# Optimization experiments

Measured on AMD Instinct MI355X. Metric: run time of the kernel, lower is better.

Reference implementation:

```python
import jax, jax.numpy as jnp
import numpy as np

B, D, OUT = 256, 512, 1024
H = (D + 1) * D // 2  # 131328 packed upper-triangular features


def setup_inputs() -> dict:
    key = jax.random.key(0)
    k1, k2 = jax.random.split(key)
    x = jax.random.normal(k1, (B, D), dtype=jnp.float32)
    # Linear weight [out_dim, halfway_dim]; original inits to zeros (learned param),
    # use small random values so the baseline output is nontrivial. bias=False.
    W = jax.random.normal(k2, (OUT, H), dtype=jnp.float32) * 0.02
    return {"x": x, "W": W}


def reference(x, W):
    d = x.shape[-1]
    iu, ju = jnp.triu_indices(d)            # static upper-tri indices (incl. diagonal)
    outer = jnp.einsum('bi,bj->bij', x, x)  # [B, D, D] per-sample outer product
    packed = outer[:, iu, ju]               # [B, H] triu gather (row-major order, matches torch bool mask)
    return packed @ W.T                     # [B, OUT] Linear, no bias
```

## Files before the change

kernel.cpp:

```cpp
#include <hip/hip_runtime.h>
#include <hip/hip_bf16.h>


#define DDIM 512
#define ODIM 1024
#define HDIM 131328L
#define NSPLIT 32
#define AST 40
#define WST 40

typedef __attribute__((ext_vector_type(4))) float floatx4;
typedef __attribute__((ext_vector_type(8))) short short8;
typedef floatx4 __attribute__((aligned(4))) floatx4u;

__device__ inline floatx4 load4u(const float* p) { return *(const floatx4u*)p; }

__device__ inline unsigned short f2bf(float v) {
    return __builtin_bit_cast(unsigned short, __float2bfloat16(v));
}

__device__ inline unsigned f2bf2(float a, float b) {
    return (unsigned)f2bf(a) | ((unsigned)f2bf(b) << 16);
}

#define BAR_PLAIN() asm volatile("s_barrier" ::: "memory")
#define BAR_LGKM()  asm volatile("s_waitcnt lgkmcnt(0)\n\ts_barrier" ::: "memory")

__global__ __launch_bounds__(512, 2) void selmul_kernel(const float* __restrict__ x,
                                                        const float* __restrict__ W,
                                                        float* __restrict__ part) {
    __shared__ __align__(16) unsigned short A_lds[256 * AST];
    __shared__ __align__(16) unsigned short W_lds[128 * WST];

    const int t    = threadIdx.x;
    const int lane = t & 63;
    const int wave = t >> 6;
    const int wm   = (wave >> 1) * 64;
    const int wn   = (wave & 1) * 64;
    const int l15  = lane & 15;
    const int quad = lane >> 4;

    const int n0 = blockIdx.x * 128;
    const int s  = blockIdx.y;

    const int c4 = t & 7;
    const int rv = t >> 3;

    floatx4 acc[4][4] = {};
    floatx4 av[4], wv[2];
    float   xi[4];

    auto mfma_phase = [&]() {
        short8 af[4], bw[4];
        #pragma unroll
        for (int fm = 0; fm < 4; ++fm)
            af[fm] = *(const short8*)&A_lds[(wm + fm * 16 + l15) * AST + quad * 8];
        #pragma unroll
        for (int fn = 0; fn < 4; ++fn)
            bw[fn] = *(const short8*)&W_lds[(wn + fn * 16 + l15) * WST + quad * 8];
        #pragma unroll
        for (int fm = 0; fm < 4; ++fm)
            #pragma unroll
            for (int fn = 0; fn < 4; ++fn)
                acc[fm][fn] = __builtin_amdgcn_mfma_f32_16x16x32_bf16(
                    af[fm], bw[fn], acc[fm][fn], 0, 0, 0);
    };

    for (int tseg = 0; tseg < 16; ++tseg) {
        const int tt   = tseg >> 1;
        const int i    = (tseg & 1) ? (63 - s + 64 * tt) : (s + 64 * tt);
        const int len  = DDIM - i;
        const long base = (long)i * DDIM - (long)i * (i - 1) / 2;
        const int full = len >> 5;
        const int rem  = len & 31;

        #pragma unroll
        for (int e = 0; e < 4; ++e)
            xi[e] = x[(rv + 64 * e) * DDIM + i];

        if (full > 0) {
            const float* axp = x + rv * DDIM + i + c4 * 4;
            const float* wpp = W + (long)(n0 + rv) * HDIM + base + c4 * 4;
            #pragma unroll
            for (int e = 0; e < 4; ++e) av[e] = load4u(axp + e * 64 * DDIM);
            #pragma unroll
            for (int e = 0; e < 2; ++e) wv[e] = load4u(wpp + (long)e * 64 * HDIM);
            axp += 32; wpp += 32;

            for (int st = 0; st < full; ++st) {
                BAR_PLAIN();
                #pragma unroll
                for (int e = 0; e < 4; ++e) {
                    const int row = rv + 64 * e;
                    floatx4 v = av[e];
                    const float sc = xi[e];
                    uint2 p;
                    p.x = f2bf2(v.x * sc, v.y * sc);
                    p.y = f2bf2(v.z * sc, v.w * sc);
                    *(uint2*)&A_lds[row * AST + c4 * 4] = p;
                }
                #pragma unroll
                for (int e = 0; e < 2; ++e) {
                    const int row = rv + 64 * e;
                    floatx4 v = wv[e];
                    uint2 p;
                    p.x = f2bf2(v.x, v.y);
                    p.y = f2bf2(v.z, v.w);
                    *(uint2*)&W_lds[row * WST + c4 * 4] = p;
                }
                if (st + 1 < full) {
                    #pragma unroll
                    for (int e = 0; e < 4; ++e) av[e] = load4u(axp + e * 64 * DDIM);
                    #pragma unroll
                    for (int e = 0; e < 2; ++e) wv[e] = load4u(wpp + (long)e * 64 * HDIM);
                    axp += 32; wpp += 32;
                }
                BAR_LGKM();
                mfma_phase();
            }
        }

        if (rem) {
            const int jj = t & 31;
            const int rb = t >> 5;
            const int j0 = i + full * 32;
            const bool valid = jj < rem;
            const int j = valid ? (j0 + jj) : i;
            const long kc = base + (long)full * 32;
            BAR_PLAIN();
            #pragma unroll
            for (int e = 0; e < 16; ++e) {
                const int m = rb + 16 * e;
                float a = valid ? x[m * DDIM + j] * x[m * DDIM + i] : 0.0f;
                A_lds[m * AST + jj] = f2bf(a);
            }
            #pragma unroll
            for (int e = 0; e < 8; ++e) {
                const int n = rb + 16 * e;
                const long ks = valid ? (kc + jj) : base;
                W_lds[n * WST + jj] = f2bf(W[(long)(n0 + n) * HDIM + ks]);
            }
            BAR_LGKM();
            mfma_phase();
        }
    }

    float* po = part + (long)s * (256 * ODIM);
    #pragma unroll
    for (int fm = 0; fm < 4; ++fm) {
        const int row = wm + fm * 16 + quad * 4;
        #pragma unroll
        for (int fn = 0; fn < 4; ++fn) {
            const int col = n0 + wn + fn * 16 + l15;
            #pragma unroll
            for (int r = 0; r < 4; ++r)
                po[(row + r) * ODIM + col] = acc[fm][fn][r];
        }
    }
}

__global__ __launch_bounds__(256) void reduce_kernel(const float* __restrict__ part,
                                                     float* __restrict__ out) {
    const int gid = blockIdx.x * 256 + threadIdx.x;
    floatx4 acc = {};
    #pragma unroll
    for (int sp = 0; sp < NSPLIT; ++sp) {
        floatx4 v = *(const floatx4*)(part + (long)sp * (256 * ODIM) + gid * 4);
        acc += v;
    }
    *(floatx4*)(out + gid * 4) = acc;
}

extern "C" void kernel_launch(void* const* d_in, const int* in_sizes, int n_in,
                              void* d_out, int out_size, void* d_ws, size_t ws_size,
                              hipStream_t stream) {
    const float* x = (const float*)d_in[0];
    const float* W = (const float*)d_in[1];
    float* out  = (float*)d_out;
    float* part = (float*)d_ws;

    hipLaunchKernelGGL(selmul_kernel, dim3(8, NSPLIT), dim3(512), 0, stream, x, W, part);
    hipLaunchKernelGGL(reduce_kernel, dim3(256), dim3(256), 0, stream, part, out);
}
```

Baseline: 852.1 us.

## Halve block N-tile to 64 and double split-K to 64 segments

Shrinks each block to 256 threads covering a 64-column output tile and splits the triangular K range across 64 row-groups instead of 32. The grid grows from 256 to 1024 blocks to raise occupancy and spread load over the MI355X CUs. The A-operand loads are now issued at the top of each K-step instead of being prefetched one step ahead. In exchange, each block recomputes the full 256-row x-outer-product tile for only 64 output columns, doubling that conversion work, and the reduce kernel must read twice as many partial buffers.

```diff
diff --git a/kernel.cpp b/kernel.cpp
--- a/kernel.cpp
+++ b/kernel.cpp
@@ -5,7 +5,8 @@
 #define DDIM 512
 #define ODIM 1024
 #define HDIM 131328L
-#define NSPLIT 32
+#define NT 16
+#define NSPLIT 64
 #define AST 40
 #define WST 40
 
@@ -18,7 +19,6 @@
 __device__ inline unsigned short f2bf(float v) {
     return __builtin_bit_cast(unsigned short, __float2bfloat16(v));
 }
-
 __device__ inline unsigned f2bf2(float a, float b) {
     return (unsigned)f2bf(a) | ((unsigned)f2bf(b) << 16);
 }
@@ -26,29 +26,28 @@
 #define BAR_PLAIN() asm volatile("s_barrier" ::: "memory")
 #define BAR_LGKM()  asm volatile("s_waitcnt lgkmcnt(0)\n\ts_barrier" ::: "memory")
 
-__global__ __launch_bounds__(512, 2) void selmul_kernel(const float* __restrict__ x,
+__global__ __launch_bounds__(256, 3) void selmul_kernel(const float* __restrict__ x,
                                                         const float* __restrict__ W,
                                                         float* __restrict__ part) {
     __shared__ __align__(16) unsigned short A_lds[256 * AST];
-    __shared__ __align__(16) unsigned short W_lds[128 * WST];
+    __shared__ __align__(16) unsigned short W_lds[64 * WST];
 
     const int t    = threadIdx.x;
     const int lane = t & 63;
     const int wave = t >> 6;
-    const int wm   = (wave >> 1) * 64;
-    const int wn   = (wave & 1) * 64;
+    const int wm   = wave * 64;
     const int l15  = lane & 15;
     const int quad = lane >> 4;
 
-    const int n0 = blockIdx.x * 128;
+    const int n0 = blockIdx.x * 64;
     const int s  = blockIdx.y;
 
     const int c4 = t & 7;
     const int rv = t >> 3;
 
     floatx4 acc[4][4] = {};
-    floatx4 av[4], wv[2];
-    float   xi[4];
+    floatx4 wv[2];
+    float   xi[8];
 
     auto mfma_phase = [&]() {
         short8 af[4], bw[4];
@@ -57,7 +56,7 @@
             af[fm] = *(const short8*)&A_lds[(wm + fm * 16 + l15) * AST + quad * 8];
         #pragma unroll
         for (int fn = 0; fn < 4; ++fn)
-            bw[fn] = *(const short8*)&W_lds[(wn + fn * 16 + l15) * WST + quad * 8];
+            bw[fn] = *(const short8*)&W_lds[(fn * 16 + l15) * WST + quad * 8];
         #pragma unroll
         for (int fm = 0; fm < 4; ++fm)
             #pragma unroll
@@ -66,54 +65,52 @@
                     af[fm], bw[fn], acc[fm][fn], 0, 0, 0);
     };
 
-    for (int tseg = 0; tseg < 16; ++tseg) {
-        const int tt   = tseg >> 1;
-        const int i    = (tseg & 1) ? (63 - s + 64 * tt) : (s + 64 * tt);
+    for (int tseg = 0; tseg < 8; ++tseg) {
+        const int t4   = tseg >> 1;
+        const int i    = (tseg & 1) ? (127 - s + 128 * t4) : (s + 128 * t4);
         const int len  = DDIM - i;
         const long base = (long)i * DDIM - (long)i * (i - 1) / 2;
         const int full = len >> 5;
         const int rem  = len & 31;
 
         #pragma unroll
-        for (int e = 0; e < 4; ++e)
-            xi[e] = x[(rv + 64 * e) * DDIM + i];
+        for (int e = 0; e < 8; ++e)
+            xi[e] = x[(rv + 32 * e) * DDIM + i];
 
         if (full > 0) {
             const float* axp = x + rv * DDIM + i + c4 * 4;
             const float* wpp = W + (long)(n0 + rv) * HDIM + base + c4 * 4;
             #pragma unroll
-            for (int e = 0; e < 4; ++e) av[e] = load4u(axp + e * 64 * DDIM);
-            #pragma unroll
-            for (int e = 0; e < 2; ++e) wv[e] = load4u(wpp + (long)e * 64 * HDIM);
-            axp += 32; wpp += 32;
+            for (int e = 0; e < 2; ++e) wv[e] = load4u(wpp + (long)e * 32 * HDIM);
+            wpp += 32;
 
             for (int st = 0; st < full; ++st) {
                 BAR_PLAIN();
+                floatx4 av[8];
                 #pragma unroll
-                for (int e = 0; e < 4; ++e) {
-                    const int row = rv + 64 * e;
+                for (int e = 0; e < 8; ++e) av[e] = load4u(axp + e * 32 * DDIM);
+                axp += 32;
+                #pragma unroll
+                for (int e = 0; e < 2; ++e) {
+                    floatx4 v = wv[e];
+                    uint2 p;
+                    p.x = f2bf2(v.x, v.y);
+                    p.y = f2bf2(v.z, v.w);
+                    *(uint2*)&W_lds[(rv + 32 * e) * WST + c4 * 4] = p;
+                }
+                if (st + 1 < full) {
+                    #pragma unroll
+                    for (int e = 0; e < 2; ++e) wv[e] = load4u(wpp + (long)e * 32 * HDIM);
+                    wpp += 32;
+                }
+                #pragma unroll
+                for (int e = 0; e < 8; ++e) {
                     floatx4 v = av[e];
                     const float sc = xi[e];
                     uint2 p;
                     p.x = f2bf2(v.x * sc, v.y * sc);
                     p.y = f2bf2(v.z * sc, v.w * sc);
-                    *(uint2*)&A_lds[row * AST + c4 * 4] = p;
-                }
-                #pragma unroll
-                for (int e = 0; e < 2; ++e) {
-                    const int row = rv + 64 * e;
-                    floatx4 v = wv[e];
-                    uint2 p;
-                    p.x = f2bf2(v.x, v.y);
-                    p.y = f2bf2(v.z, v.w);
-                    *(uint2*)&W_lds[row * WST + c4 * 4] = p;
-                }
-                if (st + 1 < full) {
-                    #pragma unroll
-                    for (int e = 0; e < 4; ++e) av[e] = load4u(axp + e * 64 * DDIM);
-                    #pragma unroll
-                    for (int e = 0; e < 2; ++e) wv[e] = load4u(wpp + (long)e * 64 * HDIM);
-                    axp += 32; wpp += 32;
+                    *(uint2*)&A_lds[(rv + 32 * e) * AST + c4 * 4] = p;
                 }
                 BAR_LGKM();
                 mfma_phase();
@@ -129,14 +126,14 @@
             const long kc = base + (long)full * 32;
             BAR_PLAIN();
             #pragma unroll
-            for (int e = 0; e < 16; ++e) {
-                const int m = rb + 16 * e;
+            for (int e = 0; e < 32; ++e) {
+                const int m = rb + 8 * e;
                 float a = valid ? x[m * DDIM + j] * x[m * DDIM + i] : 0.0f;
                 A_lds[m * AST + jj] = f2bf(a);
             }
             #pragma unroll
             for (int e = 0; e < 8; ++e) {
-                const int n = rb + 16 * e;
+                const int n = rb + 8 * e;
                 const long ks = valid ? (kc + jj) : base;
                 W_lds[n * WST + jj] = f2bf(W[(long)(n0 + n) * HDIM + ks]);
             }
@@ -151,7 +148,7 @@
         const int row = wm + fm * 16 + quad * 4;
         #pragma unroll
         for (int fn = 0; fn < 4; ++fn) {
-            const int col = n0 + wn + fn * 16 + l15;
+            const int col = n0 + fn * 16 + l15;
             #pragma unroll
             for (int r = 0; r < 4; ++r)
                 po[(row + r) * ODIM + col] = acc[fm][fn][r];
@@ -164,10 +161,8 @@
     const int gid = blockIdx.x * 256 + threadIdx.x;
     floatx4 acc = {};
     #pragma unroll
-    for (int sp = 0; sp < NSPLIT; ++sp) {
-        floatx4 v = *(const floatx4*)(part + (long)sp * (256 * ODIM) + gid * 4);
-        acc += v;
-    }
+    for (int sp = 0; sp < NSPLIT; ++sp)
+        acc += *(const floatx4*)(part + (long)sp * (256 * ODIM) + gid * 4);
     *(floatx4*)(out + gid * 4) = acc;
 }
 
@@ -179,6 +174,6 @@
     float* out  = (float*)d_out;
     float* part = (float*)d_ws;
 
-    hipLaunchKernelGGL(selmul_kernel, dim3(8, NSPLIT), dim3(512), 0, stream, x, W, part);
+    hipLaunchKernelGGL(selmul_kernel, dim3(NT, NSPLIT), dim3(256), 0, stream, x, W, part);
     hipLaunchKernelGGL(reduce_kernel, dim3(256), dim3(256), 0, stream, part, out);
 }
```

Result: slower. 918.7 us (+7.8%).
